# Kernel optimization log

Measured on AMD Instinct MI355X. Metric: run time of the kernel, lower is better.

Reference implementation:

```python
import jax, jax.numpy as jnp
import numpy as np

B, T, D = 8, 1024, 512
H = 8
F_OUT = D // H          # 64 per head
ALPHA = 0.2             # LeakyReLU slope in GAT
MASK_RATE = 0.3
GAMMA = 0.0625          # DistanceAdj gamma
BIAS = 0.2              # DistanceAdj bias
LN_EPS = 1e-5
NEG_INF = -9e15
L2_EPS = 1e-12          # F.normalize eps


def setup_inputs() -> dict:
    key = jax.random.key(0)
    ks = jax.random.split(key, 8)
    return {
        "x": jax.random.normal(ks[0], (B, T, D), jnp.float32),
        "W": jax.random.normal(ks[1], (H, D, F_OUT), jnp.float32) * 0.05,
        "a_src": jax.random.normal(ks[2], (H, F_OUT), jnp.float32) * 0.05,
        "a_dst": jax.random.normal(ks[3], (H, F_OUT), jnp.float32) * 0.05,
        "W2": jax.random.normal(ks[4], (D, D), jnp.float32) * 0.02,
        "b2": jnp.zeros((D,), jnp.float32),
        "ln_g": jnp.ones((D,), jnp.float32),
        "ln_b": jnp.zeros((D,), jnp.float32),
    }


def _distance_adj(batch, t):
    # DistanceAdj: Gaussian kernel over temporal index distance, shared across batch
    idx = jnp.arange(t, dtype=jnp.float32)
    d2 = (idx[:, None] - idx[None, :]) ** 2
    adj = jnp.exp(-GAMMA * d2 - BIAS)                      # [T, T]
    return jnp.broadcast_to(adj[None], (batch, t, t))      # [B, T, T]


def reference(x, W, a_src, a_dst, W2, b2, ln_g, ln_b):
    b, t, d = x.shape
    adj = _distance_adj(b, t)

    # top-k magnitude node selection -> row/col union mask (index_fill loop)
    k = int(MASK_RATE * t)
    mags = jnp.linalg.norm(x, axis=2)                      # [B, T]
    _, topk = jax.lax.top_k(mags, k)                       # [B, k]
    sel = jnp.zeros((b, t), bool).at[jnp.arange(b)[:, None], topk].set(True)
    mask = sel[:, :, None] | sel[:, None, :]               # rows OR cols filled
    adj = jnp.where(mask, adj, 0.0)

    # GAT multi-head attention (dense masked form, dropout=0 at eval)
    Wh = jnp.einsum("btd,hdf->bhtf", x, W)                 # [B,H,T,F']
    e_src = jnp.einsum("bhtf,hf->bht", Wh, a_src)
    e_dst = jnp.einsum("bhtf,hf->bht", Wh, a_dst)
    e = jax.nn.leaky_relu(e_src[..., :, None] + e_dst[..., None, :], ALPHA)
    e = jnp.where(adj[:, None] > 0, e, NEG_INF)            # masked logits
    attn = jax.nn.softmax(e, axis=-1)                      # [B,H,T,T]
    hp = jnp.einsum("bhts,bhsf->bhtf", attn, Wh)
    hp = jax.nn.elu(hp)                                    # concat=True -> elu per head
    tmp = hp.transpose(0, 2, 1, 3).reshape(b, t, d)        # concat heads -> [B,T,512]

    # signed-sqrt + F.normalize (default dim=1 -> over T axis)
    tmp = jnp.sqrt(jax.nn.relu(tmp)) - jnp.sqrt(jax.nn.relu(-tmp))
    nrm = jnp.linalg.norm(tmp, axis=1, keepdims=True)      # [B,1,D]
    tmp = tmp / jnp.maximum(nrm, L2_EPS)

    # residual linear + LayerNorm + permute
    y = x + tmp @ W2 + b2
    mu = jnp.mean(y, axis=-1, keepdims=True)
    var = jnp.mean((y - mu) ** 2, axis=-1, keepdims=True)
    y = (y - mu) / jnp.sqrt(var + LN_EPS) * ln_g + ln_b
    return y.transpose(0, 2, 1)                            # [B, D, T]
```

## Files before the change

kernel.cpp:

```cpp
#include <hip/hip_runtime.h>
#include <hip/hip_bf16.h>

typedef unsigned short u16;
typedef short bf16x8 __attribute__((ext_vector_type(8)));
typedef float f32x4 __attribute__((ext_vector_type(4)));
typedef int   i32x4 __attribute__((ext_vector_type(4)));

#define NB 8
#define NT 1024
#define ND 512
#define KSEL 307
#define PSTR 152
#define TSTR 136

__device__ __forceinline__ float bf2f(u16 u){
  union { unsigned int i; float f; } c; c.i = ((unsigned int)u) << 16; return c.f;
}
__device__ __forceinline__ u16 f2bf(float f){
  __hip_bfloat16 h = __float2bfloat16(f);
  u16 u; __builtin_memcpy(&u, &h, 2); return u;
}

__global__ void k_convert_w(const float* __restrict__ W, const float* __restrict__ W2,
                            u16* __restrict__ WcatT, u16* __restrict__ W2T){
  int idx = blockIdx.x * 256 + threadIdx.x;
  if (idx < 262144){
    int c = idx >> 9, d = idx & 511;
    int src = ((c >> 6) << 15) | (d << 6) | (c & 63);
    WcatT[idx] = f2bf(W[src]);
  } else {
    int i = idx - 262144;
    int n = i >> 9, k = i & 511;
    W2T[i] = f2bf(W2[(k << 9) | n]);
  }
}

__global__ void k_mags(const float* __restrict__ x, float* __restrict__ mags){
  int wid = threadIdx.x >> 6, lane = threadIdx.x & 63;
  int row = blockIdx.x * 4 + wid;
  const float* xr = x + row * ND;
  float s = 0.f;
#pragma unroll
  for (int i = 0; i < 8; i++){ float v = xr[lane + 64*i]; s += v*v; }
#pragma unroll
  for (int off = 32; off; off >>= 1) s += __shfl_xor(s, off, 64);
  if (lane == 0) mags[row] = sqrtf(s);
}

__global__ void k_select(const float* __restrict__ mags, int* __restrict__ sel){
  __shared__ float sm[NT];
  int b = blockIdx.x;
  int tid = threadIdx.x;
  for (int i = tid; i < NT; i += 256) sm[i] = mags[b * NT + i];
  __syncthreads();
  int tl = tid >> 2, tq = tid & 3;
  int t = blockIdx.y * 64 + tl;
  float m = sm[t];
  int cnt = 0;
  int s0 = tq * 256;
  for (int s = s0; s < s0 + 256; s++){
    float v = sm[s];
    cnt += (v > m) || (v == m && s < t);
  }
  cnt += __shfl_xor(cnt, 1, 64);
  cnt += __shfl_xor(cnt, 2, 64);
  if (tq == 0) sel[b * NT + t] = (cnt < KSEL) ? 1 : 0;
}

__launch_bounds__(256)
__global__ void k_gemm_wh(const float* __restrict__ x, const u16* __restrict__ Bt,
                          const float* __restrict__ a_src, const float* __restrict__ a_dst,
                          u16* __restrict__ WhT, float* __restrict__ es, float* __restrict__ ed){
  __shared__ u16 smem[128 * TSTR];
  u16* As = smem;
  u16* Bs = smem + 5120;
  int m0 = blockIdx.x * 128, n0 = blockIdx.y * 128;
  int tid = threadIdx.x;
  int wv = tid >> 6, lane = tid & 63;
  int wr = wv & 1, wc = wv >> 1;
  int quad = lane >> 4, lr = lane & 15;
  f32x4 acc[4][4] = {};
  for (int kt = 0; kt < 512; kt += 32){
    __syncthreads();
#pragma unroll
    for (int i = 0; i < 2; i++){
      int e = tid * 8 + i * 2048;
      int r = e >> 5, c = e & 31;
      const float* xa = &x[(m0 + r) * 512 + kt + c];
      f32x4 u0 = *(const f32x4*)xa;
      f32x4 u1 = *(const f32x4*)(xa + 4);
      u16 pk[8];
#pragma unroll
      for (int q = 0; q < 4; q++){ pk[q] = f2bf(u0[q]); pk[4+q] = f2bf(u1[q]); }
      *(bf16x8*)&As[r*40 + c] = *(const bf16x8*)pk;
      *(bf16x8*)&Bs[r*40 + c] = *(const bf16x8*)&Bt[(n0 + r) * 512 + kt + c];
    }
    __syncthreads();
    bf16x8 af[4], bfr[4];
#pragma unroll
    for (int i = 0; i < 4; i++){
      af[i]  = *(const bf16x8*)&As[(wr*64 + i*16 + lr)*40 + quad*8];
      bfr[i] = *(const bf16x8*)&Bs[(wc*64 + i*16 + lr)*40 + quad*8];
    }
#pragma unroll
    for (int mi = 0; mi < 4; mi++)
#pragma unroll
      for (int ni = 0; ni < 4; ni++)
        acc[mi][ni] = __builtin_amdgcn_mfma_f32_16x16x32_bf16(af[mi], bfr[ni], acc[mi][ni], 0, 0, 0);
  }
  int h = (n0 >> 6) + wc;
  float asv[4], adv[4];
#pragma unroll
  for (int ni = 0; ni < 4; ni++){
    int colg = n0 + wc*64 + ni*16 + lr;
    asv[ni] = a_src[colg & 511];
    adv[ni] = a_dst[colg & 511];
  }
#pragma unroll
  for (int mi = 0; mi < 4; mi++)
#pragma unroll
    for (int r = 0; r < 4; r++){
      float pes = 0.f, ped = 0.f;
#pragma unroll
      for (int ni = 0; ni < 4; ni++){
        pes += acc[mi][ni][r] * asv[ni];
        ped += acc[mi][ni][r] * adv[ni];
      }
#pragma unroll
      for (int mofs = 1; mofs < 16; mofs <<= 1){
        pes += __shfl_xor(pes, mofs, 64);
        ped += __shfl_xor(ped, mofs, 64);
      }
      if (lr == 0){
        int rowg = m0 + wr*64 + mi*16 + quad*4 + r;
        int bb_ = rowg >> 10, tt = rowg & 1023;
        es[(bb_ * 8 + h) * NT + tt] = pes;
        ed[(bb_ * 8 + h) * NT + tt] = ped;
      }
    }
  __syncthreads();
  u16* Tr = smem;
#pragma unroll
  for (int mi = 0; mi < 4; mi++)
#pragma unroll
    for (int ni = 0; ni < 4; ni++){
      int cl = wc*64 + ni*16 + lr;
      int tl = wr*64 + mi*16 + quad*4;
#pragma unroll
      for (int r = 0; r < 4; r++) Tr[cl*TSTR + tl + r] = f2bf(acc[mi][ni][r]);
    }
  __syncthreads();
  int c = tid >> 1, hf = tid & 1;
  int b2_ = m0 >> 10;
  u16* dst = &WhT[(b2_ * 512 + n0 + c) * NT + (m0 & 1023) + hf*64];
  const u16* srcp = &Tr[c*TSTR + hf*64];
#pragma unroll
  for (int k8 = 0; k8 < 8; k8++)
    *(bf16x8*)(dst + k8*8) = *(const bf16x8*)(srcp + k8*8);
}

__launch_bounds__(256)
__global__ void k_attn(const u16* __restrict__ WhT, const float* __restrict__ es,
                       const float* __restrict__ ed, const int* __restrict__ sel,
                       u16* __restrict__ t2b, float* __restrict__ cn){
  __shared__ u16 P[64 * PSTR];
  __shared__ float edw[144];
  __shared__ int   selw[144];
  __shared__ float esw[64];
  __shared__ float swv[64];
  int bh = blockIdx.x;
  int b = bh >> 3;
  int t0 = blockIdx.y * 64;
  int tid = threadIdx.x;
  int wv = tid >> 6, lane = tid & 63;
  int quad = lane >> 4, lr = lane & 15;
  int s_base = t0 - 40;
  for (int i = tid; i < 144; i += 256){
    int s = s_base + i;
    bool ok = (s >= 0 && s < NT);
    edw[i]  = ok ? ed[bh * NT + s] : 0.f;
    selw[i] = ok ? sel[b * NT + s] : 0;
  }
  if (tid < 64) esw[tid] = es[bh * NT + t0 + tid];
  {
    i32x4 z = {};
    for (int i = lane; i < 304; i += 64){
      int r16 = i / 19, c16 = i - r16 * 19;
      *(i32x4*)&P[(16*wv + r16) * PSTR + c16 * 8] = z;
    }
  }
  __syncthreads();
  {
    int tl = 16*wv + (lane >> 2);
    int q = lane & 3;
    float e_t = esw[tl];
    int sel_t = selw[tl + 40];
    float part = 0.f;
    for (int j = q; j <= 80; j += 4){
      int sw = tl + j;
      int s = s_base + sw;
      float w = 0.f;
      if (s >= 0 && s < NT && (sel_t | selw[sw])){
        float v = e_t + edw[sw];
        v = v > 0.f ? v : 0.2f * v;
        v = fminf(v, 60.f);
        w = bf2f(f2bf(__expf(v)));
      }
      part += w;
      if (w != 0.f) P[tl * PSTR + sw] = f2bf(w);
    }
    part += __shfl_xor(part, 1, 64);
    part += __shfl_xor(part, 2, 64);
    if (q == 0) swv[tl] = part;
  }
  f32x4 acc[4] = {};
  const u16* vbase = WhT + (bh * 64) * NT;
#pragma unroll
  for (int ks = 0; ks < 96; ks += 32){
    bf16x8 afr = *(const bf16x8*)&P[(16*wv + lr) * PSTR + 16*wv + ks + quad*8];
    int tb = s_base + 16*wv + ks + quad*8;
    bool ok = (tb >= 0) && (tb < NT);
    bf16x8 zf = {};
#pragma unroll
    for (int jn = 0; jn < 4; jn++){
      bf16x8 bfr = ok ? *(const bf16x8*)&vbase[(16*jn + lr) * NT + tb] : zf;
      acc[jn] = __builtin_amdgcn_mfma_f32_16x16x32_bf16(afr, bfr, acc[jn], 0, 0, 0);
    }
  }
#pragma unroll
  for (int jn = 0; jn < 4; jn++){
    float ssum = 0.f;
#pragma unroll
    for (int r = 0; r < 4; r++){
      int t_loc = 16*wv + quad*4 + r;
      float sw_ = swv[t_loc];
      float hp = acc[jn][r] / (sw_ > 0.f ? sw_ : 1.f);
      hp = hp > 0.f ? hp : (__expf(hp) - 1.f);
      float o = hp >= 0.f ? sqrtf(hp) : -sqrtf(-hp);
      ssum += o * o;
      t2b[(b * NT + t0 + t_loc) * ND + (bh & 7) * 64 + 16*jn + lr] = f2bf(o);
    }
    ssum += __shfl_xor(ssum, 16, 64);
    ssum += __shfl_xor(ssum, 32, 64);
    if (quad == 0) atomicAdd(&cn[b * ND + (bh & 7) * 64 + 16*jn + lr], ssum);
  }
}

__global__ void k_normalize(const u16* __restrict__ t2b, const float* __restrict__ cn,
                            u16* __restrict__ tmpb){
  int idx = (blockIdx.x * 256 + threadIdx.x) * 8;
  int b = idx >> 19;
#pragma unroll
  for (int i = 0; i < 8; i++){
    int id = idx + i;
    int d = id & 511;
    float nv = sqrtf(cn[b * ND + d]);
    float v = bf2f(t2b[id]) / fmaxf(nv, 1e-12f);
    tmpb[id] = f2bf(v);
  }
}

__launch_bounds__(256)
__global__ void k_gemm2(const u16* __restrict__ A, const u16* __restrict__ Bt,
                        const float* __restrict__ xres, const float* __restrict__ b2,
                        float* __restrict__ Y){
  __shared__ u16 As[128 * 40];
  __shared__ u16 Bs[128 * 40];
  int m0 = blockIdx.x * 128, n0 = blockIdx.y * 128;
  int tid = threadIdx.x;
  int wv = tid >> 6, lane = tid & 63;
  int wr = wv & 1, wc = wv >> 1;
  int quad = lane >> 4, lr = lane & 15;
  f32x4 acc[4][4] = {};
  for (int kt = 0; kt < 512; kt += 32){
    __syncthreads();
#pragma unroll
    for (int i = 0; i < 2; i++){
      int e = tid * 8 + i * 2048;
      int r = e >> 5, c = e & 31;
      *(bf16x8*)&As[r*40 + c] = *(const bf16x8*)&A[(m0 + r) * 512 + kt + c];
      *(bf16x8*)&Bs[r*40 + c] = *(const bf16x8*)&Bt[(n0 + r) * 512 + kt + c];
    }
    __syncthreads();
    bf16x8 af[4], bfr[4];
#pragma unroll
    for (int i = 0; i < 4; i++){
      af[i]  = *(const bf16x8*)&As[(wr*64 + i*16 + lr)*40 + quad*8];
      bfr[i] = *(const bf16x8*)&Bs[(wc*64 + i*16 + lr)*40 + quad*8];
    }
#pragma unroll
    for (int mi = 0; mi < 4; mi++)
#pragma unroll
      for (int ni = 0; ni < 4; ni++)
        acc[mi][ni] = __builtin_amdgcn_mfma_f32_16x16x32_bf16(af[mi], bfr[ni], acc[mi][ni], 0, 0, 0);
  }
#pragma unroll
  for (int mi = 0; mi < 4; mi++)
#pragma unroll
    for (int ni = 0; ni < 4; ni++){
      int rg = m0 + wr*64 + mi*16 + quad*4;
      int cg = n0 + wc*64 + ni*16 + lr;
#pragma unroll
      for (int r = 0; r < 4; r++){
        int idx = (rg + r) * 512 + cg;
        Y[idx] = acc[mi][ni][r] + xres[idx] + b2[cg];
      }
    }
}

__global__ void k_outln(const float* __restrict__ Y, const float* __restrict__ g,
                        const float* __restrict__ bb, float* __restrict__ out){
  __shared__ float mus[64], rss[64];
  __shared__ float tile[64 * 65];
  int t0 = blockIdx.x * 64, b = blockIdx.y;
  int tid = threadIdx.x;
  int wv = tid >> 6, lane = tid & 63;
  for (int i = 0; i < 16; i++){
    int row = b * NT + t0 + wv*16 + i;
    const float* yr = Y + row * ND;
    float s = 0.f, q = 0.f;
#pragma unroll
    for (int k = 0; k < 8; k++){ float v = yr[lane + 64*k]; s += v; q += v*v; }
#pragma unroll
    for (int off = 32; off; off >>= 1){ s += __shfl_xor(s, off, 64); q += __shfl_xor(q, off, 64); }
    if (lane == 0){
      float m = s * (1.f/512.f);
      float var = q * (1.f/512.f) - m * m;
      mus[wv*16 + i] = m;
      rss[wv*16 + i] = 1.f / sqrtf(var + 1e-5f);
    }
  }
  __syncthreads();
  int j = tid & 63, i0 = tid >> 6;
  for (int c0 = 0; c0 < 512; c0 += 64){
#pragma unroll
    for (int k = 0; k < 16; k++){
      int i = i0 + k * 4;
      float v = (Y[(b * NT + t0 + i) * ND + c0 + j] - mus[i]) * rss[i] * g[c0 + j] + bb[c0 + j];
      tile[i * 65 + j] = v;
    }
    __syncthreads();
#pragma unroll
    for (int k = 0; k < 16; k++){
      int jj = i0 + k * 4;
      out[(b * ND + c0 + jj) * NT + t0 + j] = tile[j * 65 + jj];
    }
    __syncthreads();
  }
}

extern "C" void kernel_launch(void* const* d_in, const int* in_sizes, int n_in,
                              void* d_out, int out_size, void* d_ws, size_t ws_size,
                              hipStream_t stream) {
  (void)in_sizes; (void)n_in; (void)out_size; (void)ws_size;
  const float* x     = (const float*)d_in[0];
  const float* W     = (const float*)d_in[1];
  const float* a_src = (const float*)d_in[2];
  const float* a_dst = (const float*)d_in[3];
  const float* W2    = (const float*)d_in[4];
  const float* b2    = (const float*)d_in[5];
  const float* ln_g  = (const float*)d_in[6];
  const float* ln_b  = (const float*)d_in[7];
  char* ws = (char*)d_ws;
  int*   sel   = (int*)  (ws + 256);
  float* mags  = (float*)(ws + 33024);
  u16*   WcatT = (u16*)  (ws + 65792);
  u16*   W2T   = (u16*)  (ws + 590080);
  float* es    = (float*)(ws + 1124608);
  float* ed    = (float*)(ws + 1386752);
  float* cn    = (float*)(ws + 1648896);
  u16*   WhT   = (u16*)  (ws + 2097152);
  u16*   t2b   = (u16*)  (ws + 18874368);
  u16*   tmpb  = t2b;
  float* Y     = (float*)(ws + 2097152);
  float* out   = (float*)d_out;

  k_mags     <<<2048, 256, 0, stream>>>(x, mags);
  k_select   <<<dim3(NB, 16), 256, 0, stream>>>(mags, sel);
  k_convert_w<<<2048, 256, 0, stream>>>(W, W2, WcatT, W2T);
  hipMemsetAsync(cn, 0, NB * ND * sizeof(float), stream);
  k_gemm_wh  <<<dim3(64, 4), 256, 0, stream>>>(x, WcatT, a_src, a_dst, WhT, es, ed);
  k_attn     <<<dim3(64, 16), 256, 0, stream>>>(WhT, es, ed, sel, t2b, cn);
  k_normalize<<<2048, 256, 0, stream>>>(t2b, cn, tmpb);
  k_gemm2    <<<dim3(64, 4), 256, 0, stream>>>(tmpb, W2T, x, b2, Y);
  k_outln    <<<dim3(16, NB), 256, 0, stream>>>(Y, ln_g, ln_b, out);
}
```

Baseline: 179.5 us.

## Fuse mags into first GEMM, normalize into second GEMM, LN stats via atomics

Three separate passes are folded into neighbouring kernels. The row-magnitude computation moves into the x-load stage of the Wh GEMM. The column normalization is applied as a per-column scale while loading A tiles in the second GEMM. The LayerNorm row sums and sums of squares are accumulated with atomics in that GEMM's epilogue. This drops three kernel launches and the extra global round trips over x, t2b and Y, at the cost of float atomics and a one-pass variance formula.

```diff
diff --git a/kernel.cpp b/kernel.cpp
--- a/kernel.cpp
+++ b/kernel.cpp
@@ -35,18 +35,6 @@
   }
 }
 
-__global__ void k_mags(const float* __restrict__ x, float* __restrict__ mags){
-  int wid = threadIdx.x >> 6, lane = threadIdx.x & 63;
-  int row = blockIdx.x * 4 + wid;
-  const float* xr = x + row * ND;
-  float s = 0.f;
-#pragma unroll
-  for (int i = 0; i < 8; i++){ float v = xr[lane + 64*i]; s += v*v; }
-#pragma unroll
-  for (int off = 32; off; off >>= 1) s += __shfl_xor(s, off, 64);
-  if (lane == 0) mags[row] = sqrtf(s);
-}
-
 __global__ void k_select(const float* __restrict__ mags, int* __restrict__ sel){
   __shared__ float sm[NT];
   int b = blockIdx.x;
@@ -70,7 +58,8 @@
 __launch_bounds__(256)
 __global__ void k_gemm_wh(const float* __restrict__ x, const u16* __restrict__ Bt,
                           const float* __restrict__ a_src, const float* __restrict__ a_dst,
-                          u16* __restrict__ WhT, float* __restrict__ es, float* __restrict__ ed){
+                          u16* __restrict__ WhT, float* __restrict__ es, float* __restrict__ ed,
+                          float* __restrict__ mags){
   __shared__ u16 smem[128 * TSTR];
   u16* As = smem;
   u16* Bs = smem + 5120;
@@ -80,6 +69,7 @@
   int wr = wv & 1, wc = wv >> 1;
   int quad = lane >> 4, lr = lane & 15;
   f32x4 acc[4][4] = {};
+  float sq[2] = {0.f, 0.f};
   for (int kt = 0; kt < 512; kt += 32){
     __syncthreads();
 #pragma unroll
@@ -91,7 +81,10 @@
       f32x4 u1 = *(const f32x4*)(xa + 4);
       u16 pk[8];
 #pragma unroll
-      for (int q = 0; q < 4; q++){ pk[q] = f2bf(u0[q]); pk[4+q] = f2bf(u1[q]); }
+      for (int q = 0; q < 4; q++){
+        sq[i] += u0[q]*u0[q] + u1[q]*u1[q];
+        pk[q] = f2bf(u0[q]); pk[4+q] = f2bf(u1[q]);
+      }
       *(bf16x8*)&As[r*40 + c] = *(const bf16x8*)pk;
       *(bf16x8*)&Bs[r*40 + c] = *(const bf16x8*)&Bt[(n0 + r) * 512 + kt + c];
     }
@@ -107,6 +100,15 @@
 #pragma unroll
       for (int ni = 0; ni < 4; ni++)
         acc[mi][ni] = __builtin_amdgcn_mfma_f32_16x16x32_bf16(af[mi], bfr[ni], acc[mi][ni], 0, 0, 0);
+  }
+  if (blockIdx.y == 0){
+#pragma unroll
+    for (int i = 0; i < 2; i++){
+      float s = sq[i];
+      s += __shfl_xor(s, 1, 64);
+      s += __shfl_xor(s, 2, 64);
+      if ((tid & 3) == 0) mags[m0 + i*64 + (tid >> 2)] = sqrtf(s);
+    }
   }
   int h = (n0 >> 6) + wc;
   float asv[4], adv[4];
@@ -246,31 +248,24 @@
   }
 }
 
-__global__ void k_normalize(const u16* __restrict__ t2b, const float* __restrict__ cn,
-                            u16* __restrict__ tmpb){
-  int idx = (blockIdx.x * 256 + threadIdx.x) * 8;
-  int b = idx >> 19;
-#pragma unroll
-  for (int i = 0; i < 8; i++){
-    int id = idx + i;
-    int d = id & 511;
-    float nv = sqrtf(cn[b * ND + d]);
-    float v = bf2f(t2b[id]) / fmaxf(nv, 1e-12f);
-    tmpb[id] = f2bf(v);
-  }
-}
-
 __launch_bounds__(256)
 __global__ void k_gemm2(const u16* __restrict__ A, const u16* __restrict__ Bt,
                         const float* __restrict__ xres, const float* __restrict__ b2,
-                        float* __restrict__ Y){
+                        const float* __restrict__ cn, float* __restrict__ Y,
+                        float* __restrict__ rsum, float* __restrict__ rqsum){
   __shared__ u16 As[128 * 40];
   __shared__ u16 Bs[128 * 40];
+  __shared__ float scl[512];
   int m0 = blockIdx.x * 128, n0 = blockIdx.y * 128;
   int tid = threadIdx.x;
   int wv = tid >> 6, lane = tid & 63;
   int wr = wv & 1, wc = wv >> 1;
   int quad = lane >> 4, lr = lane & 15;
+  int bb0 = (m0 >> 10) << 9;
+  for (int i = tid; i < 512; i += 256){
+    float nv = sqrtf(cn[bb0 + i]);
+    scl[i] = 1.f / fmaxf(nv, 1e-12f);
+  }
   f32x4 acc[4][4] = {};
   for (int kt = 0; kt < 512; kt += 32){
     __syncthreads();
@@ -278,7 +273,12 @@
     for (int i = 0; i < 2; i++){
       int e = tid * 8 + i * 2048;
       int r = e >> 5, c = e & 31;
-      *(bf16x8*)&As[r*40 + c] = *(const bf16x8*)&A[(m0 + r) * 512 + kt + c];
+      bf16x8 raw = *(const bf16x8*)&A[(m0 + r) * 512 + kt + c];
+      u16 pk[8];
+#pragma unroll
+      for (int q = 0; q < 8; q++)
+        pk[q] = f2bf(bf2f((u16)raw[q]) * scl[kt + c + q]);
+      *(bf16x8*)&As[r*40 + c] = *(const bf16x8*)pk;
       *(bf16x8*)&Bs[r*40 + c] = *(const bf16x8*)&Bt[(n0 + r) * 512 + kt + c];
     }
     __syncthreads();
@@ -294,41 +294,50 @@
       for (int ni = 0; ni < 4; ni++)
         acc[mi][ni] = __builtin_amdgcn_mfma_f32_16x16x32_bf16(af[mi], bfr[ni], acc[mi][ni], 0, 0, 0);
   }
-#pragma unroll
-  for (int mi = 0; mi < 4; mi++)
-#pragma unroll
-    for (int ni = 0; ni < 4; ni++){
-      int rg = m0 + wr*64 + mi*16 + quad*4;
-      int cg = n0 + wc*64 + ni*16 + lr;
-#pragma unroll
-      for (int r = 0; r < 4; r++){
-        int idx = (rg + r) * 512 + cg;
-        Y[idx] = acc[mi][ni][r] + xres[idx] + b2[cg];
-      }
-    }
-}
-
-__global__ void k_outln(const float* __restrict__ Y, const float* __restrict__ g,
+  float b2v[4];
+#pragma unroll
+  for (int ni = 0; ni < 4; ni++) b2v[ni] = b2[n0 + wc*64 + ni*16 + lr];
+#pragma unroll
+  for (int mi = 0; mi < 4; mi++){
+    int rgb = m0 + wr*64 + mi*16 + quad*4;
+#pragma unroll
+    for (int r = 0; r < 4; r++){
+      int row = rgb + r;
+      float rs = 0.f, rq = 0.f;
+#pragma unroll
+      for (int ni = 0; ni < 4; ni++){
+        int cg = n0 + wc*64 + ni*16 + lr;
+        int idx = row * 512 + cg;
+        float yv = acc[mi][ni][r] + xres[idx] + b2v[ni];
+        Y[idx] = yv;
+        rs += yv; rq += yv * yv;
+      }
+#pragma unroll
+      for (int m2 = 1; m2 < 16; m2 <<= 1){
+        rs += __shfl_xor(rs, m2, 64);
+        rq += __shfl_xor(rq, m2, 64);
+      }
+      if (lr == 0){
+        atomicAdd(&rsum[row], rs);
+        atomicAdd(&rqsum[row], rq);
+      }
+    }
+  }
+}
+
+__global__ void k_outln(const float* __restrict__ Y, const float* __restrict__ rsum,
+                        const float* __restrict__ rqsum, const float* __restrict__ g,
                         const float* __restrict__ bb, float* __restrict__ out){
   __shared__ float mus[64], rss[64];
   __shared__ float tile[64 * 65];
   int t0 = blockIdx.x * 64, b = blockIdx.y;
   int tid = threadIdx.x;
-  int wv = tid >> 6, lane = tid & 63;
-  for (int i = 0; i < 16; i++){
-    int row = b * NT + t0 + wv*16 + i;
-    const float* yr = Y + row * ND;
-    float s = 0.f, q = 0.f;
-#pragma unroll
-    for (int k = 0; k < 8; k++){ float v = yr[lane + 64*k]; s += v; q += v*v; }
-#pragma unroll
-    for (int off = 32; off; off >>= 1){ s += __shfl_xor(s, off, 64); q += __shfl_xor(q, off, 64); }
-    if (lane == 0){
-      float m = s * (1.f/512.f);
-      float var = q * (1.f/512.f) - m * m;
-      mus[wv*16 + i] = m;
-      rss[wv*16 + i] = 1.f / sqrtf(var + 1e-5f);
-    }
+  if (tid < 64){
+    int row = b * NT + t0 + tid;
+    float m = rsum[row] * (1.f/512.f);
+    float var = rqsum[row] * (1.f/512.f) - m * m;
+    mus[tid] = m;
+    rss[tid] = 1.f / sqrtf(var + 1e-5f);
   }
   __syncthreads();
   int j = tid & 63, i0 = tid >> 6;
@@ -369,19 +378,18 @@
   float* es    = (float*)(ws + 1124608);
   float* ed    = (float*)(ws + 1386752);
   float* cn    = (float*)(ws + 1648896);
+  float* rsum  = (float*)(ws + 1665280);
+  float* rqsum = (float*)(ws + 1698048);
   u16*   WhT   = (u16*)  (ws + 2097152);
   u16*   t2b   = (u16*)  (ws + 18874368);
-  u16*   tmpb  = t2b;
   float* Y     = (float*)(ws + 2097152);
   float* out   = (float*)d_out;
 
-  k_mags     <<<2048, 256, 0, stream>>>(x, mags);
+  k_convert_w<<<2048, 256, 0, stream>>>(W, W2, WcatT, W2T);
+  hipMemsetAsync(cn, 0, 81920, stream);
+  k_gemm_wh  <<<dim3(64, 4), 256, 0, stream>>>(x, WcatT, a_src, a_dst, WhT, es, ed, mags);
   k_select   <<<dim3(NB, 16), 256, 0, stream>>>(mags, sel);
-  k_convert_w<<<2048, 256, 0, stream>>>(W, W2, WcatT, W2T);
-  hipMemsetAsync(cn, 0, NB * ND * sizeof(float), stream);
-  k_gemm_wh  <<<dim3(64, 4), 256, 0, stream>>>(x, WcatT, a_src, a_dst, WhT, es, ed);
   k_attn     <<<dim3(64, 16), 256, 0, stream>>>(WhT, es, ed, sel, t2b, cn);
-  k_normalize<<<2048, 256, 0, stream>>>(t2b, cn, tmpb);
-  k_gemm2    <<<dim3(64, 4), 256, 0, stream>>>(tmpb, W2T, x, b2, Y);
-  k_outln    <<<dim3(16, NB), 256, 0, stream>>>(Y, ln_g, ln_b, out);
-}
+  k_gemm2    <<<dim3(64, 4), 256, 0, stream>>>(t2b, W2T, x, b2, cn, Y, rsum, rqsum);
+  k_outln    <<<dim3(16, NB), 256, 0, stream>>>(Y, rsum, rqsum, ln_g, ln_b, out);
+}
```

Result: faster. 170.0 us (-5.3%).
